# Kernel optimization log

Hardware: AMD Instinct MI355X
Metric: run time of the kernel (lower is better)

Reference implementation:

```python
import jax, jax.numpy as jnp
import numpy as np

B, DIM, IN_DIM, H, W = 4, 512, 256, 64, 64
DOWN = IN_DIM // 2          # 128
QK = DOWN // 8              # 16
EPS = 1e-5


def conv2d(x, w, b, pad=0, dil=1):
    y = jax.lax.conv_general_dilated(
        x, w, window_strides=(1, 1),
        padding=[(pad, pad), (pad, pad)],
        rhs_dilation=(dil, dil),
        dimension_numbers=('NCHW', 'OIHW', 'NCHW'))
    return y + b[None, :, None, None]


def bn(x, g, bt, m, v):
    # inference-mode BatchNorm2d with running stats
    scale = (g * jax.lax.rsqrt(v + EPS))[None, :, None, None]
    return (x - m[None, :, None, None]) * scale + bt[None, :, None, None]


def prelu(x, a):
    return jnp.where(x >= 0, x, a * x)


def setup_inputs() -> dict:
    key = jax.random.key(0)
    ks = iter(jax.random.split(key, 64))
    d = {}
    d['x'] = jax.random.normal(next(ks), (B, DIM, H, W), dtype=jnp.float32)

    def conv_params(name, cout, cin, k):
        d[name + '_w'] = jax.random.normal(next(ks), (cout, cin, k, k), jnp.float32) * 0.05
        d[name + '_b'] = jax.random.normal(next(ks), (cout,), jnp.float32) * 0.05

    def bn_params(name, c):
        d[name + '_g'] = 1.0 + 0.1 * jax.random.normal(next(ks), (c,), jnp.float32)
        d[name + '_bt'] = 0.1 * jax.random.normal(next(ks), (c,), jnp.float32)
        d[name + '_m'] = 0.1 * jax.random.normal(next(ks), (c,), jnp.float32)
        d[name + '_v'] = 0.5 + jax.random.uniform(next(ks), (c,), jnp.float32)

    def prelu_param(name):
        d[name] = jnp.full((1,), 0.25, jnp.float32)

    conv_params('dc', IN_DIM, DIM, 3);  bn_params('dc_bn', IN_DIM); prelu_param('dc_a')
    conv_params('c1', DOWN, IN_DIM, 1); bn_params('c1_bn', DOWN);   prelu_param('c1_a')
    conv_params('c2', DOWN, IN_DIM, 3); bn_params('c2_bn', DOWN);   prelu_param('c2_a')
    conv_params('q', QK, DOWN, 1)
    conv_params('k', QK, DOWN, 1)
    conv_params('v', DOWN, DOWN, 1)
    d['gamma2'] = jnp.full((1,), 0.1, jnp.float32)  # torch init is 0; nonzero to exercise the path
    conv_params('c3', DOWN, IN_DIM, 1); bn_params('c3_bn', DOWN);   prelu_param('c3_a')
    conv_params('f', IN_DIM, 3 * DOWN, 1); bn_params('f_bn', IN_DIM); prelu_param('f_a')
    return d


def reference(x,
              dc_w, dc_b, dc_bn_g, dc_bn_bt, dc_bn_m, dc_bn_v, dc_a,
              c1_w, c1_b, c1_bn_g, c1_bn_bt, c1_bn_m, c1_bn_v, c1_a,
              c2_w, c2_b, c2_bn_g, c2_bn_bt, c2_bn_m, c2_bn_v, c2_a,
              q_w, q_b, k_w, k_b, v_w, v_b, gamma2,
              c3_w, c3_b, c3_bn_g, c3_bn_bt, c3_bn_m, c3_bn_v, c3_a,
              f_w, f_b, f_bn_g, f_bn_bt, f_bn_m, f_bn_v, f_a):
    # down_conv: 3x3 conv + BN + PReLU
    x = prelu(bn(conv2d(x, dc_w, dc_b, pad=1), dc_bn_g, dc_bn_bt, dc_bn_m, dc_bn_v), dc_a)
    # branch 1: 1x1 conv
    c1 = prelu(bn(conv2d(x, c1_w, c1_b), c1_bn_g, c1_bn_bt, c1_bn_m, c1_bn_v), c1_a)
    # branch 2: dilated 3x3 conv + non-local self-attention
    c2 = prelu(bn(conv2d(x, c2_w, c2_b, pad=2, dil=2), c2_bn_g, c2_bn_bt, c2_bn_m, c2_bn_v), c2_a)
    b, c, h, w = c2.shape
    hw = h * w
    q = conv2d(c2, q_w, q_b).reshape(b, QK, hw)   # [B, C/8, HW]
    k = conv2d(c2, k_w, k_b).reshape(b, QK, hw)
    v = conv2d(c2, v_w, v_b).reshape(b, c, hw)
    energy = jnp.einsum('bcn,bcm->bnm', q, k)     # [B, HW, HW]
    attn = jax.nn.softmax(energy, axis=-1)
    out2 = jnp.einsum('bcm,bnm->bcn', v, attn).reshape(b, c, h, w)
    out2 = gamma2 * out2 + c2
    # branch 3: global avg pool -> 1x1 conv -> broadcast (bilinear upsample of 1x1 is constant)
    pooled = jnp.mean(x, axis=(2, 3), keepdims=True)  # [B, IN_DIM, 1, 1]
    c3 = prelu(bn(conv2d(pooled, c3_w, c3_b), c3_bn_g, c3_bn_bt, c3_bn_m, c3_bn_v), c3_a)
    c3 = jnp.broadcast_to(c3, (b, DOWN, h, w))
    # fuse
    cat = jnp.concatenate([c1, out2, c3], axis=1)
    return prelu(bn(conv2d(cat, f_w, f_b), f_bn_g, f_bn_bt, f_bn_m, f_bn_v), f_a)
```

## Files before the change

kernel.cpp:

```cpp
#include <hip/hip_runtime.h>
#include <hip/hip_bf16.h>
#include <math.h>

#define HW 4096
#define EPSV 1e-5f

typedef unsigned short ushort;
typedef __attribute__((ext_vector_type(8))) short bf16x8;
typedef __attribute__((ext_vector_type(4))) float f32x4;

__device__ inline ushort f2bf(float f) {
    __hip_bfloat16 h = __float2bfloat16(f);
    return *reinterpret_cast<ushort*>(&h);
}
__device__ inline float bf2f(ushort u) {
    unsigned int v = ((unsigned int)u) << 16;
    return __uint_as_float(v);
}

template<int C>
__global__ __launch_bounds__(256) void to_chlast_bf16(
    const float* __restrict__ src, ushort* __restrict__ dst)
{
    const int b = blockIdx.z, c0 = blockIdx.y * 64, p0 = blockIdx.x * 64;
    const int tid = threadIdx.x;
    __shared__ float sT[64][65];
    for (int i = tid; i < 4096; i += 256) {
        const int ch = i >> 6, px = i & 63;
        sT[ch][px] = src[(size_t)(b * C + c0 + ch) * HW + p0 + px];
    }
    __syncthreads();
    const int px = tid >> 2, seg = tid & 3;
    ushort tmp[16];
    #pragma unroll
    for (int j = 0; j < 16; ++j) tmp[j] = f2bf(sT[seg * 16 + j][px]);
    ushort* d = dst + (size_t)(b * HW + p0 + px) * C + c0 + seg * 16;
    *(uint4*)d = *(uint4*)&tmp[0];
    *(uint4*)(d + 8) = *(uint4*)&tmp[8];
}

__global__ __launch_bounds__(256) void dc_combine(
    const float* __restrict__ part,
    const float* __restrict__ bias, const float* __restrict__ bng,
    const float* __restrict__ bnb, const float* __restrict__ bnm,
    const float* __restrict__ bnv, const float* __restrict__ al,
    ushort* __restrict__ dst)
{
    const int b = blockIdx.z, c0 = blockIdx.y * 64, p0 = blockIdx.x * 64;
    const int tid = threadIdx.x;
    __shared__ float sT[64][65];
    __shared__ float sSc[64], sSh[64];
    if (tid < 64) {
        const int c = c0 + tid;
        const float sc = bng[c] * rsqrtf(bnv[c] + EPSV);
        sSc[tid] = sc;
        sSh[tid] = (bias[c] - bnm[c]) * sc + bnb[c];
    }
    __syncthreads();
    const float a = al[0];
    for (int i = tid; i < 4096; i += 256) {
        const int ch = i >> 6, px = i & 63;
        const size_t i0 = (size_t)(b * 256 + c0 + ch) * HW + p0 + px;
        float v = part[i0] + part[i0 + (size_t)4 * 256 * HW];
        float t = v * sSc[ch] + sSh[ch];
        sT[ch][px] = t >= 0.f ? t : a * t;
    }
    __syncthreads();
    const int px = tid >> 2, seg = tid & 3;
    ushort tmp[16];
    #pragma unroll
    for (int j = 0; j < 16; ++j) tmp[j] = f2bf(sT[seg * 16 + j][px]);
    ushort* d = dst + (size_t)(b * HW + p0 + px) * 256 + c0 + seg * 16;
    *(uint4*)d = *(uint4*)&tmp[0];
    *(uint4*)(d + 8) = *(uint4*)&tmp[8];
}

__global__ __launch_bounds__(256) void c2_combine(
    const float* __restrict__ part,
    const float* __restrict__ bias, const float* __restrict__ bng,
    const float* __restrict__ bnb, const float* __restrict__ bnm,
    const float* __restrict__ bnv, const float* __restrict__ al,
    float* __restrict__ out)
{
    const int c = blockIdx.y, b = blockIdx.z;
    const int px = blockIdx.x * 1024 + threadIdx.x * 4;
    const float sc = bng[c] * rsqrtf(bnv[c] + EPSV);
    const float sh = (bias[c] - bnm[c]) * sc + bnb[c];
    const float a = al[0];
    const size_t i0 = (size_t)(b * 128 + c) * HW + px;
    const float4 v0 = *(const float4*)&part[i0];
    const float4 v1 = *(const float4*)&part[i0 + (size_t)4 * 128 * HW];
    float4 o;
    float t;
    t = (v0.x + v1.x) * sc + sh; o.x = t >= 0.f ? t : a * t;
    t = (v0.y + v1.y) * sc + sh; o.y = t >= 0.f ? t : a * t;
    t = (v0.z + v1.z) * sc + sh; o.z = t >= 0.f ? t : a * t;
    t = (v0.w + v1.w) * sc + sh; o.w = t >= 0.f ? t : a * t;
    *(float4*)&out[(size_t)(b * 128 + c) * HW + px] = o;
}

template<int CIN, int COUT>
__global__ __launch_bounds__(256) void pack_w3x3(
    const float* __restrict__ w, ushort* __restrict__ wpk)
{
    const int idx = blockIdx.x * 256 + threadIdx.x;
    constexpr int total = 9 * (CIN / 32) * COUT * 32;
    if (idx >= total) return;
    const int ci_in = idx & 31;
    int rest = idx >> 5;
    const int co = rest % COUT; rest /= COUT;
    const int cc = rest % (CIN / 32);
    const int tap = rest / (CIN / 32);
    wpk[idx] = f2bf(w[((size_t)co * CIN + cc * 32 + ci_in) * 9 + tap]);
}

__global__ __launch_bounds__(256) void pack_w1x1(
    const float* __restrict__ w, ushort* __restrict__ o,
    int K, int stride, int total)
{
    const int idx = blockIdx.x * 256 + threadIdx.x;
    if (idx >= total) return;
    const int co = idx / K, k = idx - co * K;
    o[idx] = f2bf(w[(size_t)co * stride + k]);
}

template<int CIN, int COUT, int COTILE, int DIL, int ROWS, int KS>
__global__ __launch_bounds__(256) void conv3x3_mfma(
    const ushort* __restrict__ xin,
    const ushort* __restrict__ wpk,
    float* __restrict__ outp)
{
    constexpr int HR = ROWS + 2 * DIL;
    constexpr int NC = 64 + 2 * DIL;
    constexpr int MT = COTILE / 16;
    constexpr int WPR = 4 / ROWS;
    constexpr int NT = ROWS;
    constexpr int SAS = 40;
    constexpr int NCO = COUT / COTILE;
    constexpr int CH = CIN / 32 / KS;

    const int tid = threadIdx.x;
    const int wave = tid >> 6, lane = tid & 63;
    const int l15 = lane & 15, quad = lane >> 4;
    const int b = blockIdx.z;
    const int cob = blockIdx.y % NCO;
    const int ks = blockIdx.y / NCO;
    const int co0 = cob * COTILE;
    const int h0 = blockIdx.x * ROWS;
    const int row = wave / WPR;
    const int ntbase = (wave % WPR) * NT;

    __shared__ __align__(16) ushort sA[HR * NC * SAS];

    f32x4 acc[MT][NT];
    #pragma unroll
    for (int mt = 0; mt < MT; ++mt)
        #pragma unroll
        for (int nt = 0; nt < NT; ++nt) acc[mt][nt] = (f32x4){0.f, 0.f, 0.f, 0.f};

    #pragma unroll 1
    for (int cc = ks * CH; cc < (ks + 1) * CH; ++cc) {
        __syncthreads();
        constexpr int NA = HR * NC * 4;
        for (int i = tid; i < NA; i += 256) {
            const int p = i >> 2, seg = i & 3;
            const int r = p / NC, c = p - r * NC;
            const int grow = h0 - DIL + r, gcol = c - DIL;
            uint4 val = {0u, 0u, 0u, 0u};
            if (grow >= 0 && grow < 64 && gcol >= 0 && gcol < 64)
                val = *(const uint4*)&xin[((size_t)(b * 64 + grow) * 64 + gcol) * CIN
                                          + cc * 32 + seg * 8];
            *(uint4*)&sA[p * SAS + seg * 8] = val;
        }
        __syncthreads();

        #pragma unroll
        for (int ty = 0; ty < 3; ++ty)
            #pragma unroll
            for (int tx = 0; tx < 3; ++tx) {
                const int tap = ty * 3 + tx;
                bf16x8 aw[MT];
                #pragma unroll
                for (int mt = 0; mt < MT; ++mt)
                    aw[mt] = *(const bf16x8*)&wpk[
                        ((size_t)(tap * (CIN / 32) + cc) * COUT + co0 + mt * 16 + l15) * 32
                        + quad * 8];
                const int rl = row + ty * DIL;
                #pragma unroll
                for (int nt = 0; nt < NT; ++nt) {
                    const int cl = (ntbase + nt) * 16 + l15 + tx * DIL;
                    const bf16x8 bp = *(const bf16x8*)&sA[(rl * NC + cl) * SAS + quad * 8];
                    #pragma unroll
                    for (int mt = 0; mt < MT; ++mt)
                        acc[mt][nt] = __builtin_amdgcn_mfma_f32_16x16x32_bf16(
                            aw[mt], bp, acc[mt][nt], 0, 0, 0);
                }
            }
    }

    #pragma unroll
    for (int mt = 0; mt < MT; ++mt)
        #pragma unroll
        for (int rr = 0; rr < 4; ++rr) {
            const int co = co0 + mt * 16 + quad * 4 + rr;
            #pragma unroll
            for (int nt = 0; nt < NT; ++nt)
                outp[((size_t)((ks * 4 + b) * COUT + co) * 64 + h0 + row) * 64
                     + (ntbase + nt) * 16 + l15] = acc[mt][nt][rr];
        }
}

template<int CIN, int COUT, bool BNACT, int OMODE>
__global__ __launch_bounds__(256) void gemm1x1_cl(
    const ushort* __restrict__ xin,
    const ushort* __restrict__ wbf,
    const float* __restrict__ bias, const float* __restrict__ bng,
    const float* __restrict__ bnb, const float* __restrict__ bnm,
    const float* __restrict__ bnv, const float* __restrict__ al,
    const float* __restrict__ ebias, void* __restrict__ outv,
    int ostride, int ocol)
{
    const int tid = threadIdx.x;
    const int wave = tid >> 6, lane = tid & 63;
    const int l15 = lane & 15, quad = lane >> 4;
    const int pix0 = blockIdx.x * 128 + wave * 32;
    const int co0 = blockIdx.y * 64;

    f32x4 acc[4][2];
    #pragma unroll
    for (int mt = 0; mt < 4; ++mt)
        #pragma unroll
        for (int nt = 0; nt < 2; ++nt) acc[mt][nt] = (f32x4){0.f, 0.f, 0.f, 0.f};

    #pragma unroll 2
    for (int cc = 0; cc < CIN / 32; ++cc) {
        bf16x8 aw[4], bp[2];
        #pragma unroll
        for (int mt = 0; mt < 4; ++mt)
            aw[mt] = *(const bf16x8*)&wbf[(size_t)(co0 + mt * 16 + l15) * CIN + cc * 32 + quad * 8];
        #pragma unroll
        for (int nt = 0; nt < 2; ++nt)
            bp[nt] = *(const bf16x8*)&xin[(size_t)(pix0 + nt * 16 + l15) * CIN + cc * 32 + quad * 8];
        #pragma unroll
        for (int mt = 0; mt < 4; ++mt)
            #pragma unroll
            for (int nt = 0; nt < 2; ++nt)
                acc[mt][nt] = __builtin_amdgcn_mfma_f32_16x16x32_bf16(
                    aw[mt], bp[nt], acc[mt][nt], 0, 0, 0);
    }

    const int bI = pix0 >> 12;
    const float a = BNACT ? al[0] : 0.f;

    if (OMODE == 0) {
        float* out = (float*)outv;
        #pragma unroll
        for (int mt = 0; mt < 4; ++mt)
            #pragma unroll
            for (int r = 0; r < 4; ++r) {
                const int co = co0 + mt * 16 + quad * 4 + r;
                float bb = bias[co];
                if (ebias) bb += ebias[bI * COUT + co];
                float scale = 1.f, shift = bb;
                if (BNACT) {
                    scale = bng[co] * rsqrtf(bnv[co] + EPSV);
                    shift = bb * scale + (bnb[co] - bnm[co] * scale);
                }
                #pragma unroll
                for (int nt = 0; nt < 2; ++nt) {
                    float t = acc[mt][nt][r] * scale + shift;
                    if (BNACT) t = t >= 0.f ? t : a * t;
                    out[((size_t)(bI * COUT + co)) * HW + (pix0 & 4095) + nt * 16 + l15] = t;
                }
            }
    } else {
        __shared__ ushort sT[4][32][68];
        #pragma unroll
        for (int mt = 0; mt < 4; ++mt)
            #pragma unroll
            for (int r = 0; r < 4; ++r) {
                const int co = co0 + mt * 16 + quad * 4 + r;
                float bb = bias[co];
                float scale = 1.f, shift = bb;
                if (BNACT) {
                    scale = bng[co] * rsqrtf(bnv[co] + EPSV);
                    shift = bb * scale + (bnb[co] - bnm[co] * scale);
                }
                #pragma unroll
                for (int nt = 0; nt < 2; ++nt) {
                    float t = acc[mt][nt][r] * scale + shift;
                    if (BNACT) t = t >= 0.f ? t : a * t;
                    sT[wave][nt * 16 + l15][mt * 16 + quad * 4 + r] = f2bf(t);
                }
            }
        __syncthreads();
        const int p = lane >> 1, half = lane & 1;
        ushort* out = (ushort*)outv;
        #pragma unroll
        for (int seg = 0; seg < 4; ++seg) {
            uint2 a0 = *(uint2*)&sT[wave][p][half * 32 + seg * 8];
            uint2 a1 = *(uint2*)&sT[wave][p][half * 32 + seg * 8 + 4];
            uint4 vv = {a0.x, a0.y, a1.x, a1.y};
            *(uint4*)&out[(size_t)(pix0 + p) * ostride + ocol + co0 + half * 32 + seg * 8] = vv;
        }
    }
}

template<int CIN, bool BNACT, bool OUTBF16>
__global__ __launch_bounds__(256) void conv1x1_kernel(
    const float* __restrict__ in0,
    const float* __restrict__ wgt, int wstride, int COUT,
    const float* __restrict__ bias, const float* __restrict__ al,
    void* __restrict__ outv)
{
    const int tid = threadIdx.x;
    const int b = blockIdx.z, co0 = blockIdx.y * 64, p0 = blockIdx.x * 64;
    const int cg = tid >> 4, pg = tid & 15;
    const int c0l = cg * 4, w0 = pg * 4;

    __shared__ __align__(16) float sIn[16 * 64];
    __shared__ __align__(16) float sW[16 * 68];

    float acc[4][4] = {};

    for (int cc = 0; cc < CIN; cc += 16) {
        {
            int i = tid;
            #pragma unroll
            for (int it = 0; it < 4; ++it, i += 256) {
                const int px = i & 63, ci = i >> 6;
                sIn[ci * 64 + px] = in0[(size_t)(b * CIN + cc + ci) * HW + p0 + px];
            }
            i = tid;
            #pragma unroll
            for (int it = 0; it < 4; ++it, i += 256) {
                const int ci = i & 15, co = i >> 4;
                sW[ci * 68 + co] = wgt[(co0 + co) * wstride + cc + ci];
            }
        }
        __syncthreads();
        #pragma unroll
        for (int ci = 0; ci < 16; ++ci) {
            const float4 iv = *(const float4*)&sIn[ci * 64 + w0];
            const float4 wv = *(const float4*)&sW[ci * 68 + c0l];
            const float ia[4] = {iv.x, iv.y, iv.z, iv.w};
            const float wa[4] = {wv.x, wv.y, wv.z, wv.w};
            #pragma unroll
            for (int i2 = 0; i2 < 4; ++i2)
                #pragma unroll
                for (int j = 0; j < 4; ++j)
                    acc[i2][j] = fmaf(wa[i2], ia[j], acc[i2][j]);
        }
        __syncthreads();
    }

    const float a = BNACT ? al[0] : 0.f;
    #pragma unroll
    for (int i2 = 0; i2 < 4; ++i2) {
        const int co = co0 + c0l + i2;
        const float shift = bias[co];
        float r[4];
        #pragma unroll
        for (int j = 0; j < 4; ++j) {
            float t = acc[i2][j] + shift;
            r[j] = (BNACT && t < 0.f) ? a * t : t;
        }
        const size_t base = (size_t)(b * COUT + co) * HW + p0 + w0;
        if (OUTBF16) {
            ushort* out = (ushort*)outv;
            #pragma unroll
            for (int j = 0; j < 4; ++j) out[base + j] = f2bf(r[j]);
        } else {
            float* out = (float*)outv;
            *(float4*)&out[base] = make_float4(r[0], r[1], r[2], r[3]);
        }
    }
}

__global__ __launch_bounds__(256) void qk_kernel(
    const float* __restrict__ c2g, const float* __restrict__ qw,
    const float* __restrict__ qb2, const float* __restrict__ kw,
    const float* __restrict__ kb2, ushort* __restrict__ qpack,
    ushort* __restrict__ kpack)
{
    const int b = blockIdx.y, p0 = blockIdx.x * 64, tid = threadIdx.x;
    __shared__ float sC[128][64];
    __shared__ float sWq[16][128];
    __shared__ float sWk[16][128];
    for (int i = tid; i < 8192; i += 256) {
        const int px = i & 63, ci = i >> 6;
        sC[ci][px] = c2g[(size_t)(b * 128 + ci) * HW + p0 + px];
    }
    for (int i = tid; i < 2048; i += 256) {
        const int ci = i & 127, co = i >> 7;
        sWq[co][ci] = qw[co * 128 + ci];
        sWk[co][ci] = kw[co * 128 + ci];
    }
    __syncthreads();
    const int px = tid & 63, grp = tid >> 6;
    const int co0 = (grp & 1) * 8;
    const bool isK = grp >= 2;
    const float* sWp = isK ? &sWk[0][0] : &sWq[0][0];
    float acc[8] = {};
    for (int ci = 0; ci < 128; ++ci) {
        const float xv = sC[ci][px];
        #pragma unroll
        for (int j = 0; j < 8; ++j)
            acc[j] = fmaf(sWp[(co0 + j) * 128 + ci], xv, acc[j]);
    }
    const float* bsrc = isK ? kb2 : qb2;
    ushort* osrc = isK ? kpack : qpack;
    const size_t base = (size_t)(b * 4096 + p0 + px) * 32;
    #pragma unroll
    for (int j = 0; j < 8; ++j) {
        osrc[base + co0 + j] = f2bf(acc[j] + bsrc[co0 + j]);
        osrc[base + 16 + co0 + j] = 0;
    }
}

__global__ __launch_bounds__(256) void attn_flash(
    const ushort* __restrict__ qpack,
    const ushort* __restrict__ kpack,
    const ushort* __restrict__ vpackT,
    ushort* __restrict__ opart,
    float* __restrict__ Mpart,
    float* __restrict__ Spart)
{
    const int tid = threadIdx.x;
    const int wave = tid >> 6, lane = tid & 63;
    const int l15 = lane & 15, quad = lane >> 4;
    const int b = blockIdx.z, j = blockIdx.y;
    const int n0w = blockIdx.x * 128 + wave * 32;
    const int m_begin = j * 512;

    __shared__ __align__(16) ushort sV[2][128][40];
    __shared__ __align__(16) ushort sP[4][2][16][40];

    const bf16x8 bq0 = *(const bf16x8*)(qpack + ((size_t)(b * 4096 + n0w + l15) * 32 + quad * 8));
    const bf16x8 bq1 = *(const bf16x8*)(qpack + ((size_t)(b * 4096 + n0w + 16 + l15) * 32 + quad * 8));
    const f32x4 z = {0.f, 0.f, 0.f, 0.f};

    float runM0 = -3e30f, runM1 = -3e30f;
    #pragma unroll 2
    for (int t = 0; t < 8; ++t) {
        const int m0 = m_begin + t * 64;
        #pragma unroll
        for (int ms = 0; ms < 4; ++ms) {
            const bf16x8 ak = *(const bf16x8*)(
                kpack + ((size_t)(b * 4096 + m0 + ms * 16 + l15) * 32 + quad * 8));
            const f32x4 s0 = __builtin_amdgcn_mfma_f32_16x16x32_bf16(ak, bq0, z, 0, 0, 0);
            const f32x4 s1 = __builtin_amdgcn_mfma_f32_16x16x32_bf16(ak, bq1, z, 0, 0, 0);
            runM0 = fmaxf(runM0, fmaxf(fmaxf(s0[0], s0[1]), fmaxf(s0[2], s0[3])));
            runM1 = fmaxf(runM1, fmaxf(fmaxf(s1[0], s1[1]), fmaxf(s1[2], s1[3])));
        }
    }
    runM0 = fmaxf(runM0, __shfl_xor(runM0, 16));
    runM0 = fmaxf(runM0, __shfl_xor(runM0, 32));
    runM1 = fmaxf(runM1, __shfl_xor(runM1, 16));
    runM1 = fmaxf(runM1, __shfl_xor(runM1, 32));
    const float Ms0 = runM0 * 1.44269504f;
    const float Ms1 = runM1 * 1.44269504f;

    float runS0 = 0.f, runS1 = 0.f;
    f32x4 oacc0[8], oacc1[8];
    #pragma unroll
    for (int cs = 0; cs < 8; ++cs) {
        oacc0[cs] = (f32x4){0.f, 0.f, 0.f, 0.f};
        oacc1[cs] = (f32x4){0.f, 0.f, 0.f, 0.f};
    }

    const int stc = tid >> 1, stseg = tid & 1;

    {
        uint4 v0 = *(const uint4*)&vpackT[(size_t)(b * 128 + stc) * HW + m_begin + stseg * 16];
        uint4 v1 = *(const uint4*)&vpackT[(size_t)(b * 128 + stc) * HW + m_begin + stseg * 16 + 8];
        *(uint4*)&sV[0][stc][stseg * 16] = v0;
        *(uint4*)&sV[0][stc][stseg * 16 + 8] = v1;
    }
    __syncthreads();

    #pragma unroll 1
    for (int t = 0; t < 16; ++t) {
        const int m0 = m_begin + t * 32;
        const int buf = t & 1;
        uint4 nv0, nv1;
        const bool more = (t + 1 < 16);
        if (more) {
            const size_t nb = (size_t)(b * 128 + stc) * HW + m0 + 32 + stseg * 16;
            nv0 = *(const uint4*)&vpackT[nb];
            nv1 = *(const uint4*)&vpackT[nb + 8];
        }
        f32x4 s0[2], s1[2];
        #pragma unroll
        for (int ms = 0; ms < 2; ++ms) {
            const bf16x8 ak = *(const bf16x8*)(
                kpack + ((size_t)(b * 4096 + m0 + ms * 16 + l15) * 32 + quad * 8));
            s0[ms] = __builtin_amdgcn_mfma_f32_16x16x32_bf16(ak, bq0, z, 0, 0, 0);
            s1[ms] = __builtin_amdgcn_mfma_f32_16x16x32_bf16(ak, bq1, z, 0, 0, 0);
        }
        #pragma unroll
        for (int ms = 0; ms < 2; ++ms) {
            float p0[4], p1[4];
            #pragma unroll
            for (int r = 0; r < 4; ++r) {
                p0[r] = __builtin_amdgcn_exp2f(fmaf(s0[ms][r], 1.44269504f, -Ms0));
                p1[r] = __builtin_amdgcn_exp2f(fmaf(s1[ms][r], 1.44269504f, -Ms1));
                runS0 += p0[r];
                runS1 += p1[r];
            }
            ushort4 u0, u1;
            u0.x = f2bf(p0[0]); u0.y = f2bf(p0[1]); u0.z = f2bf(p0[2]); u0.w = f2bf(p0[3]);
            u1.x = f2bf(p1[0]); u1.y = f2bf(p1[1]); u1.z = f2bf(p1[2]); u1.w = f2bf(p1[3]);
            *(uint2*)&sP[wave][0][l15][ms * 16 + quad * 4] = *(uint2*)&u0;
            *(uint2*)&sP[wave][1][l15][ms * 16 + quad * 4] = *(uint2*)&u1;
        }
        asm volatile("s_waitcnt lgkmcnt(0)" ::: "memory");
        const bf16x8 ap0 = *(const bf16x8*)&sP[wave][0][l15][quad * 8];
        const bf16x8 ap1 = *(const bf16x8*)&sP[wave][1][l15][quad * 8];
        #pragma unroll
        for (int cs = 0; cs < 8; ++cs) {
            const bf16x8 bv = *(const bf16x8*)&sV[buf][cs * 16 + l15][quad * 8];
            oacc0[cs] = __builtin_amdgcn_mfma_f32_16x16x32_bf16(ap0, bv, oacc0[cs], 0, 0, 0);
            oacc1[cs] = __builtin_amdgcn_mfma_f32_16x16x32_bf16(ap1, bv, oacc1[cs], 0, 0, 0);
        }
        if (more) {
            *(uint4*)&sV[buf ^ 1][stc][stseg * 16] = nv0;
            *(uint4*)&sV[buf ^ 1][stc][stseg * 16 + 8] = nv1;
            __syncthreads();
        }
    }

    runS0 += __shfl_xor(runS0, 16);
    runS0 += __shfl_xor(runS0, 32);
    runS1 += __shfl_xor(runS1, 16);
    runS1 += __shfl_xor(runS1, 32);
    if (lane < 32) {
        const float Mv = (lane < 16) ? runM0 : runM1;
        const float Sv = (lane < 16) ? runS0 : runS1;
        const int n = n0w + ((lane < 16) ? 0 : 16) + l15;
        Mpart[((size_t)b * 8 + j) * 4096 + n] = Mv;
        Spart[((size_t)b * 8 + j) * 4096 + n] = Sv;
    }
    #pragma unroll
    for (int cs = 0; cs < 8; ++cs)
        #pragma unroll
        for (int r = 0; r < 4; ++r) {
            const int n = n0w + quad * 4 + r;
            opart[(((size_t)b * 8 + j) * 4096 + n) * 128 + cs * 16 + l15] = f2bf(oacc0[cs][r]);
            opart[(((size_t)b * 8 + j) * 4096 + n + 16) * 128 + cs * 16 + l15] = f2bf(oacc1[cs][r]);
        }
}

__global__ __launch_bounds__(256) void attn_combine(
    const ushort* __restrict__ opart, const float* __restrict__ Mpart,
    const float* __restrict__ Spart, const float* __restrict__ c2g,
    const float* __restrict__ gamma2, ushort* __restrict__ catb)
{
    const int b = blockIdx.y, n0 = blockIdx.x * 32, tid = threadIdx.x;
    __shared__ float sC2[128][33];
    __shared__ float sWj[8][32];
    if (tid < 32) {
        const int n = n0 + tid;
        float Mj[8], Sj[8];
        #pragma unroll
        for (int j = 0; j < 8; ++j) {
            Mj[j] = Mpart[((size_t)b * 8 + j) * 4096 + n];
            Sj[j] = Spart[((size_t)b * 8 + j) * 4096 + n];
        }
        float M = -3e30f;
        #pragma unroll
        for (int j = 0; j < 8; ++j) M = fmaxf(M, Mj[j]);
        float St = 0.f, e[8];
        #pragma unroll
        for (int j = 0; j < 8; ++j) { e[j] = __expf(Mj[j] - M); St += Sj[j] * e[j]; }
        const float inv = 1.0f / St;
        #pragma unroll
        for (int j = 0; j < 8; ++j) sWj[j][tid] = e[j] * inv;
    }
    #pragma unroll
    for (int e = 0; e < 16; ++e) {
        const int idx = tid + e * 256;
        const int c = idx >> 5, n = idx & 31;
        sC2[c][n] = c2g[(size_t)(b * 128 + c) * HW + n0 + n];
    }
    __syncthreads();
    const float g2 = gamma2[0];
    #pragma unroll
    for (int e = 0; e < 16; ++e) {
        const int idx = tid + e * 256;
        const int n = idx >> 7, c = idx & 127;
        float s = 0.f;
        #pragma unroll
        for (int j = 0; j < 8; ++j)
            s += bf2f(opart[(((size_t)b * 8 + j) * 4096 + n0 + n) * 128 + c]) * sWj[j][n];
        catb[(size_t)(b * 4096 + n0 + n) * 256 + 128 + c] = f2bf(fmaf(g2, s, sC2[c][n]));
    }
}

__global__ __launch_bounds__(256) void pool_kernel(
    const float* __restrict__ part,
    const float* __restrict__ bias, const float* __restrict__ bng,
    const float* __restrict__ bnb, const float* __restrict__ bnm,
    const float* __restrict__ bnv, const float* __restrict__ al,
    float* __restrict__ pool)
{
    const int c = blockIdx.x, b = blockIdx.y, tid = threadIdx.x;
    const float sc = bng[c] * rsqrtf(bnv[c] + EPSV);
    const float sh = (bias[c] - bnm[c]) * sc + bnb[c];
    const float a = al[0];
    const float4* r0 = (const float4*)(part + (size_t)(b * 256 + c) * HW);
    const float4* r1 = (const float4*)(part + (size_t)((4 + b) * 256 + c) * HW);
    float s = 0.f;
    #pragma unroll 4
    for (int i = tid; i < 1024; i += 256) {
        const float4 t0 = r0[i];
        const float4 t1 = r1[i];
        float v, t;
        v = t0.x + t1.x; t = v * sc + sh; s += t >= 0.f ? t : a * t;
        v = t0.y + t1.y; t = v * sc + sh; s += t >= 0.f ? t : a * t;
        v = t0.z + t1.z; t = v * sc + sh; s += t >= 0.f ? t : a * t;
        v = t0.w + t1.w; t = v * sc + sh; s += t >= 0.f ? t : a * t;
    }
    __shared__ float red[256];
    red[tid] = s; __syncthreads();
    for (int st = 128; st > 0; st >>= 1) {
        if (tid < st) red[tid] += red[tid + st];
        __syncthreads();
    }
    if (tid == 0) pool[b * 256 + c] = red[0] * (1.0f / 4096.0f);
}

__global__ __launch_bounds__(256) void c3_fbias_kernel(
    const float* __restrict__ pool, const float* __restrict__ c3w,
    const float* __restrict__ c3b, const float* __restrict__ bng,
    const float* __restrict__ bnb, const float* __restrict__ bnm,
    const float* __restrict__ bnv, const float* __restrict__ al,
    const float* __restrict__ fw, float* __restrict__ fbias)
{
    const int b = blockIdx.x, tid = threadIdx.x;
    __shared__ float sp[256];
    __shared__ float sc3[128];
    sp[tid] = pool[b * 256 + tid];
    __syncthreads();
    if (tid < 128) {
        float acc = c3b[tid];
        for (int ci = 0; ci < 256; ++ci) acc = fmaf(c3w[tid * 256 + ci], sp[ci], acc);
        const float scale = bng[tid] * rsqrtf(bnv[tid] + EPSV);
        float t = (acc - bnm[tid]) * scale + bnb[tid];
        const float a = al[0];
        sc3[tid] = t >= 0.f ? t : a * t;
    }
    __syncthreads();
    float f = 0.f;
    for (int j = 0; j < 128; ++j) f = fmaf(fw[tid * 384 + 256 + j], sc3[j], f);
    fbias[b * 256 + tid] = f;
}

extern "C" void kernel_launch(void* const* d_in, const int* in_sizes, int n_in,
                              void* d_out, int out_size, void* d_ws, size_t ws_size,
                              hipStream_t stream)
{
    const float* x     = (const float*)d_in[0];
    const float* dc_w  = (const float*)d_in[1];
    const float* dc_b  = (const float*)d_in[2];
    const float* dc_g  = (const float*)d_in[3];
    const float* dc_bt = (const float*)d_in[4];
    const float* dc_m  = (const float*)d_in[5];
    const float* dc_v  = (const float*)d_in[6];
    const float* dc_a  = (const float*)d_in[7];
    const float* c1_w  = (const float*)d_in[8];
    const float* c1_b  = (const float*)d_in[9];
    const float* c1_g  = (const float*)d_in[10];
    const float* c1_bt = (const float*)d_in[11];
    const float* c1_m  = (const float*)d_in[12];
    const float* c1_v  = (const float*)d_in[13];
    const float* c1_a  = (const float*)d_in[14];
    const float* c2_w  = (const float*)d_in[15];
    const float* c2_b  = (const float*)d_in[16];
    const float* c2_g  = (const float*)d_in[17];
    const float* c2_bt = (const float*)d_in[18];
    const float* c2_m  = (const float*)d_in[19];
    const float* c2_v  = (const float*)d_in[20];
    const float* c2_a  = (const float*)d_in[21];
    const float* q_w   = (const float*)d_in[22];
    const float* q_b   = (const float*)d_in[23];
    const float* k_w   = (const float*)d_in[24];
    const float* k_b   = (const float*)d_in[25];
    const float* v_w   = (const float*)d_in[26];
    const float* v_b   = (const float*)d_in[27];
    const float* gamma2= (const float*)d_in[28];
    const float* c3_w  = (const float*)d_in[29];
    const float* c3_b  = (const float*)d_in[30];
    const float* c3_g  = (const float*)d_in[31];
    const float* c3_bt = (const float*)d_in[32];
    const float* c3_m  = (const float*)d_in[33];
    const float* c3_v  = (const float*)d_in[34];
    const float* c3_a  = (const float*)d_in[35];
    const float* f_w   = (const float*)d_in[36];
    const float* f_b   = (const float*)d_in[37];
    const float* f_g   = (const float*)d_in[38];
    const float* f_bt  = (const float*)d_in[39];
    const float* f_m   = (const float*)d_in[40];
    const float* f_v   = (const float*)d_in[41];
    const float* f_a   = (const float*)d_in[42];

    char* base = (char*)d_ws;
    ushort* xbf   = (ushort*)base;
    float*  dcp   = (float*)(base + 16777216);
    ushort* opart = (ushort*)base;
    float*  c2p   = (float*)(base + 33554432);
    ushort* qpk   = (ushort*)(base + 33554432);
    ushort* kpk   = (ushort*)(base + 34603008);
    ushort* vbh   = (ushort*)(base + 35651584);
    ushort* xpbf  = (ushort*)(base + 50331648);
    float*  c2b   = (float*)(base + 50331648);
    ushort* catb  = (ushort*)(base + 58720256);
    ushort* wdcp  = (ushort*)(base + 75497472);
    ushort* wc2p  = (ushort*)(base + 77856768);
    ushort* wc1b  = (ushort*)(base + 78446592);
    ushort* wfb   = (ushort*)(base + 78512128);
    float*  poolb = (float*)(base + 78643200);
    float*  fbb   = (float*)(base + 78647296);
    float*  Mpart = (float*)(base + 78651392);
    float*  Spart = (float*)(base + 79175680);

    pack_w3x3<512, 256><<<dim3((9*16*256*32 + 255)/256), 256, 0, stream>>>(dc_w, wdcp);
    pack_w3x3<256, 128><<<dim3((9*8*128*32 + 255)/256), 256, 0, stream>>>(c2_w, wc2p);
    pack_w1x1<<<dim3((32768 + 255)/256), 256, 0, stream>>>(c1_w, wc1b, 256, 256, 32768);
    pack_w1x1<<<dim3((65536 + 255)/256), 256, 0, stream>>>(f_w, wfb, 256, 384, 65536);
    to_chlast_bf16<512><<<dim3(64, 8, 4), 256, 0, stream>>>(x, xbf);
    conv3x3_mfma<512, 256, 64, 1, 2, 2><<<dim3(32, 8, 4), 256, 0, stream>>>(
        xbf, wdcp, dcp);
    dc_combine<<<dim3(64, 4, 4), 256, 0, stream>>>(
        dcp, dc_b, dc_g, dc_bt, dc_m, dc_v, dc_a, xpbf);
    pool_kernel<<<dim3(256, 4), 256, 0, stream>>>(
        dcp, dc_b, dc_g, dc_bt, dc_m, dc_v, dc_a, poolb);
    c3_fbias_kernel<<<dim3(4), 256, 0, stream>>>(
        poolb, c3_w, c3_b, c3_g, c3_bt, c3_m, c3_v, c3_a, f_w, fbb);
    gemm1x1_cl<256, 128, true, 1><<<dim3(128, 2), 256, 0, stream>>>(
        xpbf, wc1b, c1_b, c1_g, c1_bt, c1_m, c1_v, c1_a, nullptr, catb, 256, 0);
    conv3x3_mfma<256, 128, 32, 2, 2, 2><<<dim3(32, 8, 4), 256, 0, stream>>>(
        xpbf, wc2p, c2p);
    c2_combine<<<dim3(4, 128, 4), 256, 0, stream>>>(
        c2p, c2_b, c2_g, c2_bt, c2_m, c2_v, c2_a, c2b);
    qk_kernel<<<dim3(64, 4), 256, 0, stream>>>(c2b, q_w, q_b, k_w, k_b, qpk, kpk);
    conv1x1_kernel<128, false, true><<<dim3(64, 2, 4), 256, 0, stream>>>(
        c2b, v_w, 128, 128, v_b, nullptr, vbh);
    attn_flash<<<dim3(32, 8, 4), 256, 0, stream>>>(qpk, kpk, vbh, opart, Mpart, Spart);
    attn_combine<<<dim3(128, 4), 256, 0, stream>>>(opart, Mpart, Spart, c2b, gamma2, catb);
    gemm1x1_cl<256, 256, true, 0><<<dim3(128, 4), 256, 0, stream>>>(
        catb, wfb, f_b, f_g, f_bt, f_m, f_v, f_a, fbb, (float*)d_out, 0, 0);
}
```

Before: 434.9 us.

## Prefetch next input chunk into registers and double-buffer weights in 3x3 conv

The dilated/downsample 3x3 MFMA conv now loads the next 32-channel slab of the input halo into registers while the MFMAs for the current slab run, then writes it to LDS after the compute. Weight fragments for the next tap are also fetched one tap ahead, and launch bounds request 4 blocks per SM. The goal is to hide global-memory latency behind matrix math. In exchange it uses more registers, which the occupancy hint may force into spills.

```diff
diff --git a/kernel.cpp b/kernel.cpp
--- a/kernel.cpp
+++ b/kernel.cpp
@@ -125,7 +125,7 @@
 }
 
 template<int CIN, int COUT, int COTILE, int DIL, int ROWS, int KS>
-__global__ __launch_bounds__(256) void conv3x3_mfma(
+__global__ __launch_bounds__(256, 4) void conv3x3_mfma(
     const ushort* __restrict__ xin,
     const ushort* __restrict__ wpk,
     float* __restrict__ outp)
@@ -138,6 +138,9 @@
     constexpr int SAS = 40;
     constexpr int NCO = COUT / COTILE;
     constexpr int CH = CIN / 32 / KS;
+    constexpr int NA = HR * NC * 4;
+    constexpr int NREG = (NA + 255) / 256;
+    constexpr size_t TAPSTRIDE = (size_t)(CIN / 32) * COUT * 32;
 
     const int tid = threadIdx.x;
     const int wave = tid >> 6, lane = tid & 63;
@@ -158,44 +161,93 @@
         #pragma unroll
         for (int nt = 0; nt < NT; ++nt) acc[mt][nt] = (f32x4){0.f, 0.f, 0.f, 0.f};
 
+    {
+        const int cc = ks * CH;
+        uint4 regs[NREG];
+        #pragma unroll
+        for (int k = 0; k < NREG; ++k) {
+            const int i = tid + k * 256;
+            uint4 val = {0u, 0u, 0u, 0u};
+            if (i < NA) {
+                const int p = i >> 2, seg = i & 3;
+                const int r = p / NC, c = p - r * NC;
+                const int grow = h0 - DIL + r, gcol = c - DIL;
+                if (grow >= 0 && grow < 64 && gcol >= 0 && gcol < 64)
+                    val = *(const uint4*)&xin[((size_t)(b * 64 + grow) * 64 + gcol) * CIN
+                                              + cc * 32 + seg * 8];
+            }
+            regs[k] = val;
+        }
+        #pragma unroll
+        for (int k = 0; k < NREG; ++k) {
+            const int i = tid + k * 256;
+            if (i < NA) *(uint4*)&sA[(i >> 2) * SAS + (i & 3) * 8] = regs[k];
+        }
+        __syncthreads();
+    }
+
     #pragma unroll 1
     for (int cc = ks * CH; cc < (ks + 1) * CH; ++cc) {
-        __syncthreads();
-        constexpr int NA = HR * NC * 4;
-        for (int i = tid; i < NA; i += 256) {
-            const int p = i >> 2, seg = i & 3;
-            const int r = p / NC, c = p - r * NC;
-            const int grow = h0 - DIL + r, gcol = c - DIL;
-            uint4 val = {0u, 0u, 0u, 0u};
-            if (grow >= 0 && grow < 64 && gcol >= 0 && gcol < 64)
-                val = *(const uint4*)&xin[((size_t)(b * 64 + grow) * 64 + gcol) * CIN
-                                          + cc * 32 + seg * 8];
-            *(uint4*)&sA[p * SAS + seg * 8] = val;
-        }
-        __syncthreads();
-
-        #pragma unroll
-        for (int ty = 0; ty < 3; ++ty)
-            #pragma unroll
-            for (int tx = 0; tx < 3; ++tx) {
-                const int tap = ty * 3 + tx;
-                bf16x8 aw[MT];
+        const bool more = (cc + 1 < (ks + 1) * CH);
+
+        const ushort* wb = wpk + ((size_t)cc * COUT + co0 + l15) * 32 + quad * 8;
+        bf16x8 awc[MT];
+        #pragma unroll
+        for (int mt = 0; mt < MT; ++mt)
+            awc[mt] = *(const bf16x8*)&wb[mt * 512];
+
+        uint4 regs[NREG];
+        if (more) {
+            #pragma unroll
+            for (int k = 0; k < NREG; ++k) {
+                const int i = tid + k * 256;
+                uint4 val = {0u, 0u, 0u, 0u};
+                if (i < NA) {
+                    const int p = i >> 2, seg = i & 3;
+                    const int r = p / NC, c = p - r * NC;
+                    const int grow = h0 - DIL + r, gcol = c - DIL;
+                    if (grow >= 0 && grow < 64 && gcol >= 0 && gcol < 64)
+                        val = *(const uint4*)&xin[((size_t)(b * 64 + grow) * 64 + gcol) * CIN
+                                                  + (cc + 1) * 32 + seg * 8];
+                }
+                regs[k] = val;
+            }
+        }
+
+        #pragma unroll
+        for (int tap = 0; tap < 9; ++tap) {
+            bf16x8 awn[MT];
+            if (tap < 8) {
                 #pragma unroll
                 for (int mt = 0; mt < MT; ++mt)
-                    aw[mt] = *(const bf16x8*)&wpk[
-                        ((size_t)(tap * (CIN / 32) + cc) * COUT + co0 + mt * 16 + l15) * 32
-                        + quad * 8];
-                const int rl = row + ty * DIL;
+                    awn[mt] = *(const bf16x8*)&wb[(size_t)(tap + 1) * TAPSTRIDE + mt * 512];
+            }
+            const int ty = tap / 3, tx = tap - ty * 3;
+            const int rl = row + ty * DIL;
+            #pragma unroll
+            for (int nt = 0; nt < NT; ++nt) {
+                const int cl = (ntbase + nt) * 16 + l15 + tx * DIL;
+                const bf16x8 bp = *(const bf16x8*)&sA[(rl * NC + cl) * SAS + quad * 8];
                 #pragma unroll
-                for (int nt = 0; nt < NT; ++nt) {
-                    const int cl = (ntbase + nt) * 16 + l15 + tx * DIL;
-                    const bf16x8 bp = *(const bf16x8*)&sA[(rl * NC + cl) * SAS + quad * 8];
-                    #pragma unroll
-                    for (int mt = 0; mt < MT; ++mt)
-                        acc[mt][nt] = __builtin_amdgcn_mfma_f32_16x16x32_bf16(
-                            aw[mt], bp, acc[mt][nt], 0, 0, 0);
-                }
-            }
+                for (int mt = 0; mt < MT; ++mt)
+                    acc[mt][nt] = __builtin_amdgcn_mfma_f32_16x16x32_bf16(
+                        awc[mt], bp, acc[mt][nt], 0, 0, 0);
+            }
+            if (tap < 8) {
+                #pragma unroll
+                for (int mt = 0; mt < MT; ++mt) awc[mt] = awn[mt];
+            }
+        }
+
+        if (more) {
+            __syncthreads();
+            #pragma unroll
+            for (int k = 0; k < NREG; ++k) {
+                const int i = tid + k * 256;
+                if (i < NA) *(uint4*)&sA[(i >> 2) * SAS + (i & 3) * 8] = regs[k];
+            }
+            __syncthreads();
+        }
     }
 
     #pragma unroll
```

New measurement: 428.8 us. No clear change (-1.4%).

## Stage conv3x3 weights in LDS and stream activations from global memory

Applied to the files above, without the earlier changes.

Swaps which operand of the 3x3 MFMA convolution goes through shared memory. Weights for each 32-channel chunk are prefetched into registers one chunk ahead and written to LDS, while activation fragments are read straight from global memory per tap, with a one-tap software prefetch. This removes the halo-tile LDS fill and its index arithmetic, and adds an occupancy hint to launch bounds. The risk is more uncached-looking global traffic, since each input pixel is re-read for every tap and wave instead of being reused from LDS.

```diff
diff --git a/kernel.cpp b/kernel.cpp
--- a/kernel.cpp
+++ b/kernel.cpp
@@ -125,19 +125,18 @@
 }
 
 template<int CIN, int COUT, int COTILE, int DIL, int ROWS, int KS>
-__global__ __launch_bounds__(256) void conv3x3_mfma(
+__global__ __launch_bounds__(256, 4) void conv3x3_mfma(
     const ushort* __restrict__ xin,
     const ushort* __restrict__ wpk,
     float* __restrict__ outp)
 {
-    constexpr int HR = ROWS + 2 * DIL;
-    constexpr int NC = 64 + 2 * DIL;
     constexpr int MT = COTILE / 16;
     constexpr int WPR = 4 / ROWS;
     constexpr int NT = ROWS;
-    constexpr int SAS = 40;
     constexpr int NCO = COUT / COTILE;
     constexpr int CH = CIN / 32 / KS;
+    constexpr int WCH = 9 * MT * 64;
+    constexpr int WPT = (WCH + 255) / 256;
 
     const int tid = threadIdx.x;
     const int wave = tid >> 6, lane = tid & 63;
@@ -150,52 +149,91 @@
     const int row = wave / WPR;
     const int ntbase = (wave % WPR) * NT;
 
-    __shared__ __align__(16) ushort sA[HR * NC * SAS];
+    __shared__ __align__(16) ushort sW[WCH * 8];
 
     f32x4 acc[MT][NT];
     #pragma unroll
     for (int mt = 0; mt < MT; ++mt)
         #pragma unroll
         for (int nt = 0; nt < NT; ++nt) acc[mt][nt] = (f32x4){0.f, 0.f, 0.f, 0.f};
+
+    const int grow_base = h0 + row - DIL;
+
+    uint4 wreg[WPT];
+    auto loadw = [&](int ccw) {
+        #pragma unroll
+        for (int k2 = 0; k2 < WPT; ++k2) {
+            const int i = tid + k2 * 256;
+            if (i < WCH) {
+                const int tap = i / (MT * 64);
+                const int r = i - tap * (MT * 64);
+                const int mt = r >> 6, n = r & 63;
+                wreg[k2] = *(const uint4*)&wpk[
+                    ((size_t)(tap * (CIN / 32) + ccw) * COUT + co0 + mt * 16 + (n & 15)) * 32
+                    + (n >> 4) * 8];
+            }
+        }
+    };
+
+    loadw(ks * CH);
 
     #pragma unroll 1
     for (int cc = ks * CH; cc < (ks + 1) * CH; ++cc) {
+        const bool more = (cc + 1 < (ks + 1) * CH);
+
+        if (cc != ks * CH) __syncthreads();
+        #pragma unroll
+        for (int k2 = 0; k2 < WPT; ++k2) {
+            const int i = tid + k2 * 256;
+            if (i < WCH) *(uint4*)&sW[i * 8] = wreg[k2];
+        }
         __syncthreads();
-        constexpr int NA = HR * NC * 4;
-        for (int i = tid; i < NA; i += 256) {
-            const int p = i >> 2, seg = i & 3;
-            const int r = p / NC, c = p - r * NC;
-            const int grow = h0 - DIL + r, gcol = c - DIL;
-            uint4 val = {0u, 0u, 0u, 0u};
-            if (grow >= 0 && grow < 64 && gcol >= 0 && gcol < 64)
-                val = *(const uint4*)&xin[((size_t)(b * 64 + grow) * 64 + gcol) * CIN
-                                          + cc * 32 + seg * 8];
-            *(uint4*)&sA[p * SAS + seg * 8] = val;
-        }
-        __syncthreads();
-
-        #pragma unroll
-        for (int ty = 0; ty < 3; ++ty)
-            #pragma unroll
-            for (int tx = 0; tx < 3; ++tx) {
-                const int tap = ty * 3 + tx;
-                bf16x8 aw[MT];
+
+        if (more) loadw(cc + 1);
+
+        bf16x8 bcur[NT], bnext[NT];
+        {
+            const int gr = grow_base;
+            #pragma unroll
+            for (int nt = 0; nt < NT; ++nt) {
+                const int gc = (ntbase + nt) * 16 + l15 - DIL;
+                bf16x8 v = {0, 0, 0, 0, 0, 0, 0, 0};
+                if (gr >= 0 && gr < 64 && gc >= 0 && gc < 64)
+                    v = *(const bf16x8*)&xin[((size_t)(b * 64 + gr) * 64 + gc) * CIN
+                                             + cc * 32 + quad * 8];
+                bcur[nt] = v;
+            }
+        }
+        #pragma unroll
+        for (int tap = 0; tap < 9; ++tap) {
+            if (tap < 8) {
+                const int tyn = (tap + 1) / 3, txn = (tap + 1) - tyn * 3;
+                const int gr = grow_base + tyn * DIL;
+                #pragma unroll
+                for (int nt = 0; nt < NT; ++nt) {
+                    const int gc = (ntbase + nt) * 16 + l15 + (txn - 1) * DIL;
+                    bf16x8 v = {0, 0, 0, 0, 0, 0, 0, 0};
+                    if (gr >= 0 && gr < 64 && gc >= 0 && gc < 64)
+                        v = *(const bf16x8*)&xin[((size_t)(b * 64 + gr) * 64 + gc) * CIN
+                                                 + cc * 32 + quad * 8];
+                    bnext[nt] = v;
+                }
+            }
+            bf16x8 wf[MT];
+            #pragma unroll
+            for (int mt = 0; mt < MT; ++mt)
+                wf[mt] = *(const bf16x8*)&sW[((tap * MT + mt) * 64 + lane) * 8];
+            #pragma unroll
+            for (int nt = 0; nt < NT; ++nt)
                 #pragma unroll
                 for (int mt = 0; mt < MT; ++mt)
-                    aw[mt] = *(const bf16x8*)&wpk[
-                        ((size_t)(tap * (CIN / 32) + cc) * COUT + co0 + mt * 16 + l15) * 32
-                        + quad * 8];
-                const int rl = row + ty * DIL;
+                    acc[mt][nt] = __builtin_amdgcn_mfma_f32_16x16x32_bf16(
+                        wf[mt], bcur[nt], acc[mt][nt], 0, 0, 0);
+            if (tap < 8) {
                 #pragma unroll
-                for (int nt = 0; nt < NT; ++nt) {
-                    const int cl = (ntbase + nt) * 16 + l15 + tx * DIL;
-                    const bf16x8 bp = *(const bf16x8*)&sA[(rl * NC + cl) * SAS + quad * 8];
-                    #pragma unroll
-                    for (int mt = 0; mt < MT; ++mt)
-                        acc[mt][nt] = __builtin_amdgcn_mfma_f32_16x16x32_bf16(
-                            aw[mt], bp, acc[mt][nt], 0, 0, 0);
-                }
-            }
+                for (int nt = 0; nt < NT; ++nt) bcur[nt] = bnext[nt];
+            }
+        }
     }
 
     #pragma unroll
```

Measured after the change: 528.2 us. 1.21x slower.

## Stage conv3x3 weights in LDS, prefetch next channel chunk into registers, retile

Applied to the files above, without the earlier changes.

The 3x3 MFMA convolution now stages each channel chunk's weights in shared memory rather than loading them from global memory per tap. It also prefetches the next chunk's activations and weights into registers while the current chunk computes, a software double-buffer. Tile shapes change: four rows per block and a larger c2 output-channel tile, with split-K raised to 4 for the c2 conv. The c2 partial buffer moves to the workspace base, and c2_combine is templated to sum a variable number of partials. This aims to hide global-load latency and cut redundant weight traffic, at the cost of more registers and LDS and extra partial-sum traffic for c2.

```diff
diff --git a/kernel.cpp b/kernel.cpp
--- a/kernel.cpp
+++ b/kernel.cpp
@@ -75,6 +75,7 @@
     *(uint4*)(d + 8) = *(uint4*)&tmp[8];
 }
 
+template<int KS>
 __global__ __launch_bounds__(256) void c2_combine(
     const float* __restrict__ part,
     const float* __restrict__ bias, const float* __restrict__ bng,
@@ -88,14 +89,18 @@
     const float sh = (bias[c] - bnm[c]) * sc + bnb[c];
     const float a = al[0];
     const size_t i0 = (size_t)(b * 128 + c) * HW + px;
-    const float4 v0 = *(const float4*)&part[i0];
-    const float4 v1 = *(const float4*)&part[i0 + (size_t)4 * 128 * HW];
+    float4 s = {0.f, 0.f, 0.f, 0.f};
+    #pragma unroll
+    for (int k = 0; k < KS; ++k) {
+        const float4 v = *(const float4*)&part[i0 + (size_t)k * 4 * 128 * HW];
+        s.x += v.x; s.y += v.y; s.z += v.z; s.w += v.w;
+    }
     float4 o;
     float t;
-    t = (v0.x + v1.x) * sc + sh; o.x = t >= 0.f ? t : a * t;
-    t = (v0.y + v1.y) * sc + sh; o.y = t >= 0.f ? t : a * t;
-    t = (v0.z + v1.z) * sc + sh; o.z = t >= 0.f ? t : a * t;
-    t = (v0.w + v1.w) * sc + sh; o.w = t >= 0.f ? t : a * t;
+    t = s.x * sc + sh; o.x = t >= 0.f ? t : a * t;
+    t = s.y * sc + sh; o.y = t >= 0.f ? t : a * t;
+    t = s.z * sc + sh; o.z = t >= 0.f ? t : a * t;
+    t = s.w * sc + sh; o.w = t >= 0.f ? t : a * t;
     *(float4*)&out[(size_t)(b * 128 + c) * HW + px] = o;
 }
 
@@ -125,7 +130,7 @@
 }
 
 template<int CIN, int COUT, int COTILE, int DIL, int ROWS, int KS>
-__global__ __launch_bounds__(256) void conv3x3_mfma(
+__global__ __launch_bounds__(256, 2) void conv3x3_mfma(
     const ushort* __restrict__ xin,
     const ushort* __restrict__ wpk,
     float* __restrict__ outp)
@@ -138,6 +143,10 @@
     constexpr int SAS = 40;
     constexpr int NCO = COUT / COTILE;
     constexpr int CH = CIN / 32 / KS;
+    constexpr int NA = HR * NC * 4;
+    constexpr int NREG = (NA + 255) / 256;
+    constexpr int WCH = 9 * MT * 64;
+    constexpr int WPT = (WCH + 255) / 256;
 
     const int tid = threadIdx.x;
     const int wave = tid >> 6, lane = tid & 63;
@@ -151,51 +160,89 @@
     const int ntbase = (wave % WPR) * NT;
 
     __shared__ __align__(16) ushort sA[HR * NC * SAS];
+    __shared__ __align__(16) ushort sW[WCH * 8];
 
     f32x4 acc[MT][NT];
     #pragma unroll
     for (int mt = 0; mt < MT; ++mt)
         #pragma unroll
         for (int nt = 0; nt < NT; ++nt) acc[mt][nt] = (f32x4){0.f, 0.f, 0.f, 0.f};
+
+    uint4 xreg[NREG];
+    uint4 wreg[WPT];
+
+    auto loadx = [&](int cc) {
+        #pragma unroll
+        for (int k = 0; k < NREG; ++k) {
+            const int i = tid + k * 256;
+            uint4 val = {0u, 0u, 0u, 0u};
+            if (i < NA) {
+                const int p = i >> 2, seg = i & 3;
+                const int r = p / NC, c = p - r * NC;
+                const int grow = h0 - DIL + r, gcol = c - DIL;
+                if (grow >= 0 && grow < 64 && gcol >= 0 && gcol < 64)
+                    val = *(const uint4*)&xin[((size_t)(b * 64 + grow) * 64 + gcol) * CIN
+                                              + cc * 32 + seg * 8];
+            }
+            xreg[k] = val;
+        }
+    };
+    auto loadw = [&](int cc) {
+        #pragma unroll
+        for (int k = 0; k < WPT; ++k) {
+            const int i = tid + k * 256;
+            if (i < WCH) {
+                const int tap = i / (MT * 64);
+                const int r = i - tap * (MT * 64);
+                const int mt = r >> 6, n = r & 63;
+                wreg[k] = *(const uint4*)&wpk[
+                    ((size_t)(tap * (CIN / 32) + cc) * COUT + co0 + mt * 16 + (n & 15)) * 32
+                    + (n >> 4) * 8];
+            }
+        }
+    };
+
+    loadx(ks * CH);
+    loadw(ks * CH);
 
     #pragma unroll 1
     for (int cc = ks * CH; cc < (ks + 1) * CH; ++cc) {
+        if (cc != ks * CH) __syncthreads();
+        #pragma unroll
+        for (int k = 0; k < NREG; ++k) {
+            const int i = tid + k * 256;
+            if (i < NA) *(uint4*)&sA[(i >> 2) * SAS + (i & 3) * 8] = xreg[k];
+        }
+        #pragma unroll
+        for (int k = 0; k < WPT; ++k) {
+            const int i = tid + k * 256;
+            if (i < WCH) *(uint4*)&sW[i * 8] = wreg[k];
+        }
         __syncthreads();
-        constexpr int NA = HR * NC * 4;
-        for (int i = tid; i < NA; i += 256) {
-            const int p = i >> 2, seg = i & 3;
-            const int r = p / NC, c = p - r * NC;
-            const int grow = h0 - DIL + r, gcol = c - DIL;
-            uint4 val = {0u, 0u, 0u, 0u};
-            if (grow >= 0 && grow < 64 && gcol >= 0 && gcol < 64)
-                val = *(const uint4*)&xin[((size_t)(b * 64 + grow) * 64 + gcol) * CIN
-                                          + cc * 32 + seg * 8];
-            *(uint4*)&sA[p * SAS + seg * 8] = val;
-        }
-        __syncthreads();
-
-        #pragma unroll
-        for (int ty = 0; ty < 3; ++ty)
-            #pragma unroll
-            for (int tx = 0; tx < 3; ++tx) {
-                const int tap = ty * 3 + tx;
-                bf16x8 aw[MT];
+
+        if (cc + 1 < (ks + 1) * CH) {
+            loadx(cc + 1);
+            loadw(cc + 1);
+        }
+
+        #pragma unroll
+        for (int tap = 0; tap < 9; ++tap) {
+            const int ty = tap / 3, tx = tap - ty * 3;
+            const int rl = row + ty * DIL;
+            bf16x8 wf[MT];
+            #pragma unroll
+            for (int mt = 0; mt < MT; ++mt)
+                wf[mt] = *(const bf16x8*)&sW[((tap * MT + mt) * 64 + lane) * 8];
+            #pragma unroll
+            for (int nt = 0; nt < NT; ++nt) {
+                const int cl = (ntbase + nt) * 16 + l15 + tx * DIL;
+                const bf16x8 bp = *(const bf16x8*)&sA[(rl * NC + cl) * SAS + quad * 8];
                 #pragma unroll
                 for (int mt = 0; mt < MT; ++mt)
-                    aw[mt] = *(const bf16x8*)&wpk[
-                        ((size_t)(tap * (CIN / 32) + cc) * COUT + co0 + mt * 16 + l15) * 32
-                        + quad * 8];
-                const int rl = row + ty * DIL;
-                #pragma unroll
-                for (int nt = 0; nt < NT; ++nt) {
-                    const int cl = (ntbase + nt) * 16 + l15 + tx * DIL;
-                    const bf16x8 bp = *(const bf16x8*)&sA[(rl * NC + cl) * SAS + quad * 8];
-                    #pragma unroll
-                    for (int mt = 0; mt < MT; ++mt)
-                        acc[mt][nt] = __builtin_amdgcn_mfma_f32_16x16x32_bf16(
-                            aw[mt], bp, acc[mt][nt], 0, 0, 0);
-                }
+                    acc[mt][nt] = __builtin_amdgcn_mfma_f32_16x16x32_bf16(
+                        wf[mt], bp, acc[mt][nt], 0, 0, 0);
             }
+        }
     }
 
     #pragma unroll
@@ -707,8 +754,8 @@
     char* base = (char*)d_ws;
     ushort* xbf   = (ushort*)base;
     float*  dcp   = (float*)(base + 16777216);
+    float*  c2p   = (float*)base;
     ushort* opart = (ushort*)base;
-    float*  c2p   = (float*)(base + 33554432);
     ushort* qpk   = (ushort*)(base + 33554432);
     ushort* kpk   = (ushort*)(base + 34603008);
     ushort* vbh   = (ushort*)(base + 35651584);
@@ -729,7 +776,7 @@
     pack_w1x1<<<dim3((32768 + 255)/256), 256, 0, stream>>>(c1_w, wc1b, 256, 256, 32768);
     pack_w1x1<<<dim3((65536 + 255)/256), 256, 0, stream>>>(f_w, wfb, 256, 384, 65536);
     to_chlast_bf16<512><<<dim3(64, 8, 4), 256, 0, stream>>>(x, xbf);
-    conv3x3_mfma<512, 256, 64, 1, 2, 2><<<dim3(32, 8, 4), 256, 0, stream>>>(
+    conv3x3_mfma<512, 256, 64, 1, 4, 2><<<dim3(16, 8, 4), 256, 0, stream>>>(
         xbf, wdcp, dcp);
     dc_combine<<<dim3(64, 4, 4), 256, 0, stream>>>(
         dcp, dc_b, dc_g, dc_bt, dc_m, dc_v, dc_a, xpbf);
@@ -739,9 +786,9 @@
         poolb, c3_w, c3_b, c3_g, c3_bt, c3_m, c3_v, c3_a, f_w, fbb);
     gemm1x1_cl<256, 128, true, 1><<<dim3(128, 2), 256, 0, stream>>>(
         xpbf, wc1b, c1_b, c1_g, c1_bt, c1_m, c1_v, c1_a, nullptr, catb, 256, 0);
-    conv3x3_mfma<256, 128, 32, 2, 2, 2><<<dim3(32, 8, 4), 256, 0, stream>>>(
+    conv3x3_mfma<256, 128, 64, 2, 4, 4><<<dim3(16, 8, 4), 256, 0, stream>>>(
         xpbf, wc2p, c2p);
-    c2_combine<<<dim3(4, 128, 4), 256, 0, stream>>>(
+    c2_combine<4><<<dim3(4, 128, 4), 256, 0, stream>>>(
         c2p, c2_b, c2_g, c2_bt, c2_m, c2_v, c2_a, c2b);
     qk_kernel<<<dim3(64, 4), 256, 0, stream>>>(c2b, q_w, q_b, k_w, k_b, qpk, kpk);
     conv1x1_kernel<128, false, true><<<dim3(64, 2, 4), 256, 0, stream>>>(
```

Measured after the change: 418.6 us. -3.7%, faster.
